# Kernel tuning notes

Measured on AMD Instinct MI355X. Metric: run time of the kernel, lower is better.

## Reference

```python
import jax, jax.numpy as jnp
import numpy as np

N = 50000
E = 800000
F_IN = 256
HID = 96
N_CLS = 32
NEG_SLOPE = 0.2


def setup_inputs() -> dict:
    key = jax.random.key(0)
    ks = jax.random.split(key, 10)
    x = jax.random.normal(ks[0], (N, F_IN), dtype=jnp.float32)
    edge_index = jax.random.randint(ks[1], (2, E), 0, N, dtype=jnp.int64)
    s1 = 1.0 / np.sqrt(F_IN)
    s2 = 1.0 / np.sqrt(HID)
    return {
        "x": x,
        "edge_index": edge_index,
        "W1": jax.random.normal(ks[2], (F_IN, HID), dtype=jnp.float32) * s1,
        "a1_src": jax.random.normal(ks[3], (HID,), dtype=jnp.float32) * s2,
        "a1_dst": jax.random.normal(ks[4], (HID,), dtype=jnp.float32) * s2,
        "b1": jnp.zeros((HID,), dtype=jnp.float32),
        "W2": jax.random.normal(ks[5], (HID, N_CLS), dtype=jnp.float32) * s2,
        "a2_src": jax.random.normal(ks[6], (N_CLS,), dtype=jnp.float32) * (1.0 / np.sqrt(N_CLS)),
        "a2_dst": jax.random.normal(ks[7], (N_CLS,), dtype=jnp.float32) * (1.0 / np.sqrt(N_CLS)),
        "b2": jnp.zeros((N_CLS,), dtype=jnp.float32),
    }


def _gat_conv(x, src, dst, W, a_src, a_dst, b, n_nodes):
    # single-head GATConv (PyG defaults), self-loops already in src/dst
    h = x @ W                                  # [N, out]
    alpha_src = h @ a_src                      # [N]
    alpha_dst = h @ a_dst                      # [N]
    e = alpha_src[src] + alpha_dst[dst]        # [E'] edge logits (msg j->i: dst groups)
    e = jnp.where(e > 0, e, NEG_SLOPE * e)     # leaky_relu
    # segment softmax over edges grouped by destination node
    m = jax.ops.segment_max(e, dst, num_segments=n_nodes)
    ex = jnp.exp(e - m[dst])
    denom = jax.ops.segment_sum(ex, dst, num_segments=n_nodes)
    alpha = ex / denom[dst]                    # [E']
    out = jax.ops.segment_sum(alpha[:, None] * h[src], dst, num_segments=n_nodes)
    return out + b


def reference(x, edge_index, W1, a1_src, a1_dst, b1, W2, a2_src, a2_dst, b2):
    loops = jnp.arange(N, dtype=edge_index.dtype)
    src = jnp.concatenate([edge_index[0], loops])
    dst = jnp.concatenate([edge_index[1], loops])
    h = _gat_conv(x, src, dst, W1, a1_src, a1_dst, b1, N)
    h = jax.nn.elu(h)
    # dropout omitted (eval mode, training=False)
    out = _gat_conv(h, src, dst, W2, a2_src, a2_dst, b2, N)
    return jax.nn.log_softmax(out, axis=1)
```

## Files before the change

kernel.cpp:

```cpp
#include <hip/hip_runtime.h>
#include <cstdint>
#include <cstddef>

#define NNODES 50000
#define NEDGES 800000
#define MEDGES (NEDGES + NNODES)
#define FIN    256
#define HID    96
#define NCLS   32
#define NEG_SLOPE 0.2f

#define NBUCK  391
#define BCAP   3072

typedef unsigned int uint32;
typedef __attribute__((ext_vector_type(8))) short short8;
typedef __attribute__((ext_vector_type(4))) float f32x4;

__device__ __forceinline__ ushort bf_round(float f) {
    uint32 u = __float_as_uint(f);
    u += 0x7FFFu + ((u >> 16) & 1u);
    return (ushort)(u >> 16);
}
__device__ __forceinline__ float bf_lo(uint32 u) { return __uint_as_float(u << 16); }
__device__ __forceinline__ float bf_hi(uint32 u) { return __uint_as_float(u & 0xFFFF0000u); }
__device__ __forceinline__ float lrelu(float t) { return (t > 0.f) ? t : NEG_SLOPE * t; }


__global__ __launch_bounds__(256) void bucket1_kernel(const int* __restrict__ ei,
                                                      int* __restrict__ gcount,
                                                      int2* __restrict__ staging) {
    __shared__ int hist[NBUCK];
    __shared__ int base_sh[NBUCK];
    for (int i = threadIdx.x; i < NBUCK; i += 256) hist[i] = 0;
    __syncthreads();

    int s[8], d[8], rk[8], bk[8];
    int e0 = blockIdx.x * 2048;
#pragma unroll
    for (int i = 0; i < 8; ++i) {
        int e = e0 + i * 256 + threadIdx.x;
        if (e < MEDGES) {
            if (e < NEDGES) { s[i] = ei[e]; d[i] = ei[NEDGES + e]; }
            else            { s[i] = e - NEDGES; d[i] = s[i]; }
            bk[i] = d[i] >> 7;
            rk[i] = atomicAdd(&hist[bk[i]], 1);
        } else bk[i] = -1;
    }
    __syncthreads();
    for (int i = threadIdx.x; i < NBUCK; i += 256) {
        int c = hist[i];
        base_sh[i] = c ? atomicAdd(&gcount[i], c) : 0;
    }
    __syncthreads();
#pragma unroll
    for (int i = 0; i < 8; ++i) {
        if (bk[i] >= 0) {
            int pos = base_sh[bk[i]] + rk[i];
            if (pos < BCAP)
                staging[(size_t)bk[i] * BCAP + pos] = make_int2(s[i], d[i]);
        }
    }
}

__global__ __launch_bounds__(512) void bscan_kernel(const int* __restrict__ gcount,
                                                    int* __restrict__ bbase) {
    __shared__ int sd[512];
    int t = threadIdx.x;
    int v = (t < NBUCK) ? gcount[t] : 0;
    sd[t] = v;
    __syncthreads();
    for (int off = 1; off < 512; off <<= 1) {
        int val = (t >= off) ? sd[t - off] : 0;
        __syncthreads();
        sd[t] += val;
        __syncthreads();
    }
    if (t < NBUCK) bbase[t] = sd[t] - v;
}

__global__ __launch_bounds__(256) void bucket2_kernel(const int2* __restrict__ staging,
                                                      const int* __restrict__ gcount,
                                                      const int* __restrict__ bbase,
                                                      int* __restrict__ rowptr,
                                                      int* __restrict__ esrc) {
    __shared__ int dcount[128];
    __shared__ int dincl[128];
    __shared__ int dexcl[128];
    __shared__ int fillc[128];

    const int b     = blockIdx.x;
    const int t     = threadIdx.x;
    const int cnt   = gcount[b];
    const int ebase = bbase[b];
    const int node0 = b << 7;
    const int2* st  = staging + (size_t)b * BCAP;

    for (int i = t; i < 128; i += 256) { dcount[i] = 0; fillc[i] = 0; }
    __syncthreads();

    for (int i = t; i < cnt; i += 256)
        atomicAdd(&dcount[st[i].y - node0], 1);
    __syncthreads();

    if (t < 128) dincl[t] = dcount[t];
    __syncthreads();
    for (int off = 1; off < 128; off <<= 1) {
        int val = (t >= off && t < 128) ? dincl[t - off] : 0;
        __syncthreads();
        if (t < 128) dincl[t] += val;
        __syncthreads();
    }
    if (t < 128) {
        int excl = dincl[t] - dcount[t];
        dexcl[t] = excl;
        int node = node0 + t;
        if (node < NNODES) rowptr[node] = ebase + excl;
    }
    if (b == NBUCK - 1 && t == 0) rowptr[NNODES] = MEDGES;
    __syncthreads();

    for (int i = t; i < cnt; i += 256) {
        int2 sd2 = st[i];
        int dd = sd2.y - node0;
        int r = atomicAdd(&fillc[dd], 1);
        esrc[ebase + dexcl[dd] + r] = sd2.x;
    }
}


__global__ __launch_bounds__(256) void packw1_kernel(const float* __restrict__ W1,
                                                     ushort* __restrict__ W1p) {
    for (int idx = threadIdx.x; idx < 6 * 8 * 64 * 8; idx += 256) {
        int j     = idx & 7;
        int lane  = (idx >> 3) & 63;
        int kstep = (idx >> 9) & 7;
        int ntile = idx >> 12;
        int k = kstep * 32 + ((lane >> 4) << 3) + j;
        int n = ntile * 16 + (lane & 15);
        W1p[idx] = bf_round(W1[(size_t)k * 96 + n]);
    }
}


__global__ __launch_bounds__(256) void gemm1_kernel(const float* __restrict__ x,
                                                    const ushort* __restrict__ W1p,
                                                    const float* __restrict__ a_src,
                                                    const float* __restrict__ a_dst,
                                                    ushort* __restrict__ h1,
                                                    float* __restrict__ as1,
                                                    float* __restrict__ ad1) {
    const int tid  = threadIdx.x;
    const int lane = tid & 63;
    const int wv   = tid >> 6;
    const int m    = lane & 15;
    const int quad = lane >> 4;
    const int node0 = blockIdx.x * 64;

    int arow = node0 + wv * 16 + m;
    if (arow >= NNODES) arow = NNODES - 1;
    const float* xr = x + (size_t)arow * FIN + quad * 8;

    const short8* Wp = (const short8*)W1p;

    f32x4 acc[6];
#pragma unroll
    for (int t = 0; t < 6; ++t) acc[t] = (f32x4){0.f, 0.f, 0.f, 0.f};

#pragma unroll
    for (int ks = 0; ks < 8; ++ks) {
        float4 v0 = *(const float4*)(xr + ks * 32);
        float4 v1 = *(const float4*)(xr + ks * 32 + 4);
        short8 a;
        a[0] = (short)bf_round(v0.x); a[1] = (short)bf_round(v0.y);
        a[2] = (short)bf_round(v0.z); a[3] = (short)bf_round(v0.w);
        a[4] = (short)bf_round(v1.x); a[5] = (short)bf_round(v1.y);
        a[6] = (short)bf_round(v1.z); a[7] = (short)bf_round(v1.w);
#pragma unroll
        for (int t = 0; t < 6; ++t) {
            short8 b = Wp[(t * 8 + ks) * 64 + lane];
            acc[t] = __builtin_amdgcn_mfma_f32_16x16x32_bf16(a, b, acc[t], 0, 0, 0);
        }
    }

    float as_reg[6], ad_reg[6];
#pragma unroll
    for (int t = 0; t < 6; ++t) {
        as_reg[t] = a_src[t * 16 + m];
        ad_reg[t] = a_dst[t * 16 + m];
    }

#pragma unroll
    for (int r = 0; r < 4; ++r) {
        int node = node0 + wv * 16 + quad * 4 + r;
        float ps = 0.f, pd = 0.f;
#pragma unroll
        for (int t = 0; t < 6; ++t) {
            ps += acc[t][r] * as_reg[t];
            pd += acc[t][r] * ad_reg[t];
        }
#pragma unroll
        for (int off = 1; off < 16; off <<= 1) {
            ps += __shfl_xor(ps, off);
            pd += __shfl_xor(pd, off);
        }
        if (node < NNODES) {
            ushort* hp = h1 + (size_t)node * 96 + m;
#pragma unroll
            for (int t = 0; t < 6; ++t) hp[t * 16] = bf_round(acc[t][r]);
            if (m == 0) { as1[node] = ps; ad1[node] = pd; }
        }
    }
}


__global__ __launch_bounds__(256) void gemm2_kernel(const float* __restrict__ y,
                                                    const float* __restrict__ W2,
                                                    const float* __restrict__ a_src,
                                                    const float* __restrict__ a_dst,
                                                    float* __restrict__ h2,
                                                    float* __restrict__ as2,
                                                    float* __restrict__ ad2) {
    __shared__ float ysT[96][66];
    __shared__ float red[2][4][64];

    const int tid  = threadIdx.x;
    const int lane = tid & 63;
    const int wid  = __builtin_amdgcn_readfirstlane(tid >> 6);
    const int node0 = blockIdx.x * 64;
    const int node  = node0 + lane;

    const int sr = tid & 63;
    const int sc = tid >> 6;
    int srow = node0 + sr; if (srow >= NNODES) srow = NNODES - 1;
    const float* yr = y + (size_t)srow * HID;

#pragma unroll
    for (int i = 0; i < 6; ++i) {
        int c = sc + 4 * i;
        float4 v = *(const float4*)(yr + 4 * c);
        int k = 4 * c;
        ysT[k + 0][sr] = v.x;
        ysT[k + 1][sr] = v.y;
        ysT[k + 2][sr] = v.z;
        ysT[k + 3][sr] = v.w;
    }
    __syncthreads();

    float acc[8];
#pragma unroll
    for (int j = 0; j < 8; ++j) acc[j] = 0.f;

#pragma unroll 4
    for (int k = 0; k < HID; ++k) {
        float xv = ysT[k][lane];
        const float* wr = W2 + (size_t)k * 32 + wid * 8;
        float w[8];
#pragma unroll
        for (int j = 0; j < 8; ++j) w[j] = wr[j];
#pragma unroll
        for (int j = 0; j < 8; ++j) acc[j] = fmaf(xv, w[j], acc[j]);
    }

    float ps = 0.f, pd = 0.f;
#pragma unroll
    for (int j = 0; j < 8; ++j) {
        ps += acc[j] * a_src[wid * 8 + j];
        pd += acc[j] * a_dst[wid * 8 + j];
    }
    red[0][wid][lane] = ps;
    red[1][wid][lane] = pd;

    if (node < NNODES) {
        float* hp = h2 + (size_t)node * NCLS + wid * 8;
        *(float4*)(hp + 0) = make_float4(acc[0], acc[1], acc[2], acc[3]);
        *(float4*)(hp + 4) = make_float4(acc[4], acc[5], acc[6], acc[7]);
    }
    __syncthreads();
    if (tid < 64) {
        int n2 = node0 + tid;
        if (n2 < NNODES) {
            as2[n2] = red[0][0][tid] + red[0][1][tid] + red[0][2][tid] + red[0][3][tid];
            ad2[n2] = red[1][0][tid] + red[1][1][tid] + red[1][2][tid] + red[1][3][tid];
        }
    }
}


__global__ __launch_bounds__(256) void agg96_kernel(const ushort* __restrict__ h,
                                                    const float* __restrict__ asrc,
                                                    const float* __restrict__ adst,
                                                    const float* __restrict__ bias,
                                                    const int* __restrict__ rowptr,
                                                    const int* __restrict__ esrc,
                                                    float* __restrict__ out) {
    int wave = threadIdx.x >> 6;
    int lane = threadIdx.x & 63;
    int i = blockIdx.x * 4 + wave;
    if (i >= NNODES) return;

    int start = rowptr[i], end = rowptr[i + 1];
    int deg = end - start;
    float ad = adst[i];
    int fl = (lane < 48) ? lane : 47;

    float acc0 = 0.f, acc1 = 0.f;

    if (deg <= 64) {
        int p = start + lane;
        bool valid = p < end;
        int s_reg = valid ? esrc[p] : 0;
        float e = -1e30f;
        if (valid) e = lrelu(asrc[s_reg] + ad);
        float mx = e;
#pragma unroll
        for (int off = 32; off; off >>= 1) mx = fmaxf(mx, __shfl_xor(mx, off));
        float ex = valid ? __expf(e - mx) : 0.f;
        float sum = ex;
#pragma unroll
        for (int off = 32; off; off >>= 1) sum += __shfl_xor(sum, off);
        float a_reg = ex / sum;

        int main_end = deg & ~3;
        for (int eb = 0; eb < main_end; eb += 4) {
            int s0 = __shfl(s_reg, eb + 0), s1 = __shfl(s_reg, eb + 1);
            int s2 = __shfl(s_reg, eb + 2), s3 = __shfl(s_reg, eb + 3);
            float a0 = __shfl(a_reg, eb + 0), a1 = __shfl(a_reg, eb + 1);
            float a2 = __shfl(a_reg, eb + 2), a3 = __shfl(a_reg, eb + 3);
            uint32 u0 = ((const uint32*)(h + (size_t)s0 * 96))[fl];
            uint32 u1 = ((const uint32*)(h + (size_t)s1 * 96))[fl];
            uint32 u2 = ((const uint32*)(h + (size_t)s2 * 96))[fl];
            uint32 u3 = ((const uint32*)(h + (size_t)s3 * 96))[fl];
            acc0 += a0 * bf_lo(u0) + a1 * bf_lo(u1) + a2 * bf_lo(u2) + a3 * bf_lo(u3);
            acc1 += a0 * bf_hi(u0) + a1 * bf_hi(u1) + a2 * bf_hi(u2) + a3 * bf_hi(u3);
        }
        for (int e2 = main_end; e2 < deg; ++e2) {
            int s = __shfl(s_reg, e2);
            float a = __shfl(a_reg, e2);
            uint32 u = ((const uint32*)(h + (size_t)s * 96))[fl];
            acc0 += a * bf_lo(u);
            acc1 += a * bf_hi(u);
        }
    } else {
        float mx = -1e30f;
        for (int p = start + lane; p < end; p += 64)
            mx = fmaxf(mx, lrelu(asrc[esrc[p]] + ad));
#pragma unroll
        for (int off = 32; off; off >>= 1) mx = fmaxf(mx, __shfl_xor(mx, off));
        float sum = 0.f;
        for (int p = start + lane; p < end; p += 64)
            sum += __expf(lrelu(asrc[esrc[p]] + ad) - mx);
#pragma unroll
        for (int off = 32; off; off >>= 1) sum += __shfl_xor(sum, off);
        float inv = 1.f / sum;
        for (int p = start; p < end; ++p) {
            int s = esrc[p];
            float a = __expf(lrelu(asrc[s] + ad) - mx) * inv;
            uint32 u = ((const uint32*)(h + (size_t)s * 96))[fl];
            acc0 += a * bf_lo(u);
            acc1 += a * bf_hi(u);
        }
    }

    if (lane < 48) {
        float v0 = acc0 + bias[2 * lane];
        v0 = (v0 > 0.f) ? v0 : expm1f(v0);
        float v1 = acc1 + bias[2 * lane + 1];
        v1 = (v1 > 0.f) ? v1 : expm1f(v1);
        *(float2*)(out + (size_t)i * 96 + 2 * lane) = make_float2(v0, v1);
    }
}


__global__ __launch_bounds__(256) void agg32_kernel(const float* __restrict__ h,
                                                    const float* __restrict__ asrc,
                                                    const float* __restrict__ adst,
                                                    const float* __restrict__ bias,
                                                    const int* __restrict__ rowptr,
                                                    const int* __restrict__ esrc,
                                                    float* __restrict__ out) {
    int wave = threadIdx.x >> 6;
    int lane = threadIdx.x & 63;
    int i = blockIdx.x * 4 + wave;
    if (i >= NNODES) return;

    int e2 = lane >> 5;
    int f  = lane & 31;

    int start = rowptr[i], end = rowptr[i + 1];
    int deg = end - start;
    float ad = adst[i];

    float acc = 0.f;

    if (deg <= 64) {
        int p = start + lane;
        bool valid = p < end;
        int s_reg = valid ? esrc[p] : 0;
        float e = -1e30f;
        if (valid) e = lrelu(asrc[s_reg] + ad);
        float mx = e;
#pragma unroll
        for (int off = 32; off; off >>= 1) mx = fmaxf(mx, __shfl_xor(mx, off));
        float ex = valid ? __expf(e - mx) : 0.f;
        float sum = ex;
#pragma unroll
        for (int off = 32; off; off >>= 1) sum += __shfl_xor(sum, off);
        float a_reg = ex / sum;

        int main_end = deg & ~7;
        for (int eb = 0; eb < main_end; eb += 8) {
            int idx0 = eb + e2, idx1 = eb + e2 + 2, idx2 = eb + e2 + 4, idx3 = eb + e2 + 6;
            int s0 = __shfl(s_reg, idx0), s1 = __shfl(s_reg, idx1);
            int s2 = __shfl(s_reg, idx2), s3 = __shfl(s_reg, idx3);
            float a0 = __shfl(a_reg, idx0), a1 = __shfl(a_reg, idx1);
            float a2 = __shfl(a_reg, idx2), a3 = __shfl(a_reg, idx3);
            float v0 = h[(size_t)s0 * 32 + f];
            float v1 = h[(size_t)s1 * 32 + f];
            float v2 = h[(size_t)s2 * 32 + f];
            float v3 = h[(size_t)s3 * 32 + f];
            acc += a0 * v0 + a1 * v1 + a2 * v2 + a3 * v3;
        }
        for (int e3 = main_end + e2; e3 < deg; e3 += 2) {
            int s = __shfl(s_reg, e3);
            float a = __shfl(a_reg, e3);
            acc += a * h[(size_t)s * 32 + f];
        }
        acc += __shfl_xor(acc, 32);
    } else {
        float mx = -1e30f;
        for (int p = start + lane; p < end; p += 64)
            mx = fmaxf(mx, lrelu(asrc[esrc[p]] + ad));
#pragma unroll
        for (int off = 32; off; off >>= 1) mx = fmaxf(mx, __shfl_xor(mx, off));
        float sum = 0.f;
        for (int p = start + lane; p < end; p += 64)
            sum += __expf(lrelu(asrc[esrc[p]] + ad) - mx);
#pragma unroll
        for (int off = 32; off; off >>= 1) sum += __shfl_xor(sum, off);
        float inv = 1.f / sum;
        for (int p = start + e2; p < end; p += 2) {
            int s = esrc[p];
            float a = __expf(lrelu(asrc[s] + ad) - mx) * inv;
            acc += a * h[(size_t)s * 32 + f];
        }
        acc += __shfl_xor(acc, 32);
    }

    float z = acc + bias[f];
    float m2 = z;
#pragma unroll
    for (int off = 16; off; off >>= 1) m2 = fmaxf(m2, __shfl_xor(m2, off));
    float ex = __expf(z - m2);
    float s2 = ex;
#pragma unroll
    for (int off = 16; off; off >>= 1) s2 += __shfl_xor(s2, off);
    if (lane < 32) out[(size_t)i * 32 + f] = z - m2 - logf(s2);
}


extern "C" void kernel_launch(void* const* d_in, const int* in_sizes, int n_in,
                              void* d_out, int out_size, void* d_ws, size_t ws_size,
                              hipStream_t stream) {
    const float* x   = (const float*)d_in[0];
    const int*   ei  = (const int*)d_in[1];
    const float* W1  = (const float*)d_in[2];
    const float* a1s = (const float*)d_in[3];
    const float* a1d = (const float*)d_in[4];
    const float* b1  = (const float*)d_in[5];
    const float* W2  = (const float*)d_in[6];
    const float* a2s = (const float*)d_in[7];
    const float* a2d = (const float*)d_in[8];
    const float* b2  = (const float*)d_in[9];
    float* out = (float*)d_out;

    size_t off = 0;
    auto alloc = [&](size_t bytes) {
        void* p = (char*)d_ws + off;
        off += (bytes + 255) & ~(size_t)255;
        return p;
    };
    ushort* h1    = (ushort*)alloc((size_t)NNODES * HID * 2);
    float* out1   = (float*)alloc((size_t)NNODES * HID * 4);
    int2* staging = (int2*)alloc((size_t)NBUCK * BCAP * 8);
    float* as1    = (float*)alloc((size_t)NNODES * 4);
    float* ad1    = (float*)alloc((size_t)NNODES * 4);
    float* as2    = (float*)alloc((size_t)NNODES * 4);
    float* ad2    = (float*)alloc((size_t)NNODES * 4);
    int*   rowptr = (int*)alloc((size_t)(NNODES + 1) * 4);
    int*   esrc   = (int*)alloc((size_t)MEDGES * 4);
    ushort* W1p   = (ushort*)alloc((size_t)6 * 8 * 64 * 8 * 2);
    int*   gcount = (int*)alloc((size_t)NBUCK * 4);
    int*   bbase  = (int*)alloc((size_t)NBUCK * 4);
    float* h2     = (float*)h1;

    hipMemsetAsync(gcount, 0, (size_t)NBUCK * 4, stream);

    const int nbB1   = (MEDGES + 2047) / 2048;
    const int nbGemm = (NNODES + 63) / 64;
    const int nbAgg  = (NNODES + 3) / 4;

    packw1_kernel<<<1, 256, 0, stream>>>(W1, W1p);
    bucket1_kernel<<<nbB1, 256, 0, stream>>>(ei, gcount, staging);
    bscan_kernel<<<1, 512, 0, stream>>>(gcount, bbase);
    bucket2_kernel<<<NBUCK, 256, 0, stream>>>(staging, gcount, bbase, rowptr, esrc);

    gemm1_kernel<<<nbGemm, 256, 0, stream>>>(x, W1p, a1s, a1d, h1, as1, ad1);
    agg96_kernel<<<nbAgg, 256, 0, stream>>>(h1, as1, ad1, b1, rowptr, esrc, out1);

    gemm2_kernel<<<nbGemm, 256, 0, stream>>>(out1, W2, a2s, a2d, h2, as2, ad2);
    agg32_kernel<<<nbAgg, 256, 0, stream>>>(h2, as2, ad2, b2, rowptr, esrc, out);
}
```

Baseline: 244.5 us.

## Store layer-1 output as bf16, use MFMA for GEMM2, stage edge weights in LDS

The first aggregation now writes its ELU output as packed bf16 instead of fp32, which halves that intermediate's write and read traffic. The second GEMM switches from a scalar LDS-transposed FMA loop to bf16 MFMA 16x16x32, with W2 pre-packed into fragment layout by the shared pack kernel. Both aggregation kernels place per-edge (src, alpha) pairs in LDS and read them with vector loads instead of repeated cross-lane shuffles, and agg96 unrolls its gather loop by 8. The cost is more bf16 rounding on the hidden activations and in the second GEMM.

```diff
diff --git a/kernel.cpp b/kernel.cpp
--- a/kernel.cpp
+++ b/kernel.cpp
@@ -22,9 +22,13 @@
     u += 0x7FFFu + ((u >> 16) & 1u);
     return (ushort)(u >> 16);
 }
+__device__ __forceinline__ uint32 pack_bf16x2(float a, float b) {
+    return (uint32)bf_round(a) | ((uint32)bf_round(b) << 16);
+}
 __device__ __forceinline__ float bf_lo(uint32 u) { return __uint_as_float(u << 16); }
 __device__ __forceinline__ float bf_hi(uint32 u) { return __uint_as_float(u & 0xFFFF0000u); }
 __device__ __forceinline__ float lrelu(float t) { return (t > 0.f) ? t : NEG_SLOPE * t; }
+__device__ __forceinline__ float af(int i) { return __int_as_float(i); }
 
 
 __global__ __launch_bounds__(256) void bucket1_kernel(const int* __restrict__ ei,
@@ -129,8 +133,10 @@
 }
 
 
-__global__ __launch_bounds__(256) void packw1_kernel(const float* __restrict__ W1,
-                                                     ushort* __restrict__ W1p) {
+__global__ __launch_bounds__(256) void packw_kernel(const float* __restrict__ W1,
+                                                    const float* __restrict__ W2,
+                                                    ushort* __restrict__ W1p,
+                                                    ushort* __restrict__ W2p) {
     for (int idx = threadIdx.x; idx < 6 * 8 * 64 * 8; idx += 256) {
         int j     = idx & 7;
         int lane  = (idx >> 3) & 63;
@@ -139,6 +145,15 @@
         int k = kstep * 32 + ((lane >> 4) << 3) + j;
         int n = ntile * 16 + (lane & 15);
         W1p[idx] = bf_round(W1[(size_t)k * 96 + n]);
+    }
+    for (int idx = threadIdx.x; idx < 2 * 3 * 64 * 8; idx += 256) {
+        int j     = idx & 7;
+        int lane  = (idx >> 3) & 63;
+        int kstep = (idx >> 9) % 3;
+        int ntile = (idx >> 9) / 3;
+        int k = kstep * 32 + ((lane >> 4) << 3) + j;
+        int n = ntile * 16 + (lane & 15);
+        W2p[idx] = bf_round(W2[(size_t)k * 32 + n]);
     }
 }
 
@@ -214,74 +229,65 @@
 }
 
 
-__global__ __launch_bounds__(256) void gemm2_kernel(const float* __restrict__ y,
-                                                    const float* __restrict__ W2,
+__global__ __launch_bounds__(256) void gemm2_kernel(const uint32* __restrict__ y48,
+                                                    const ushort* __restrict__ W2p,
                                                     const float* __restrict__ a_src,
                                                     const float* __restrict__ a_dst,
                                                     float* __restrict__ h2,
                                                     float* __restrict__ as2,
                                                     float* __restrict__ ad2) {
-    __shared__ float ysT[96][66];
-    __shared__ float red[2][4][64];
-
     const int tid  = threadIdx.x;
     const int lane = tid & 63;
-    const int wid  = __builtin_amdgcn_readfirstlane(tid >> 6);
+    const int wv   = tid >> 6;
+    const int m    = lane & 15;
+    const int quad = lane >> 4;
     const int node0 = blockIdx.x * 64;
-    const int node  = node0 + lane;
-
-    const int sr = tid & 63;
-    const int sc = tid >> 6;
-    int srow = node0 + sr; if (srow >= NNODES) srow = NNODES - 1;
-    const float* yr = y + (size_t)srow * HID;
-
-#pragma unroll
-    for (int i = 0; i < 6; ++i) {
-        int c = sc + 4 * i;
-        float4 v = *(const float4*)(yr + 4 * c);
-        int k = 4 * c;
-        ysT[k + 0][sr] = v.x;
-        ysT[k + 1][sr] = v.y;
-        ysT[k + 2][sr] = v.z;
-        ysT[k + 3][sr] = v.w;
-    }
-    __syncthreads();
-
-    float acc[8];
-#pragma unroll
-    for (int j = 0; j < 8; ++j) acc[j] = 0.f;
-
-#pragma unroll 4
-    for (int k = 0; k < HID; ++k) {
-        float xv = ysT[k][lane];
-        const float* wr = W2 + (size_t)k * 32 + wid * 8;
-        float w[8];
-#pragma unroll
-        for (int j = 0; j < 8; ++j) w[j] = wr[j];
-#pragma unroll
-        for (int j = 0; j < 8; ++j) acc[j] = fmaf(xv, w[j], acc[j]);
-    }
-
-    float ps = 0.f, pd = 0.f;
-#pragma unroll
-    for (int j = 0; j < 8; ++j) {
-        ps += acc[j] * a_src[wid * 8 + j];
-        pd += acc[j] * a_dst[wid * 8 + j];
-    }
-    red[0][wid][lane] = ps;
-    red[1][wid][lane] = pd;
-
-    if (node < NNODES) {
-        float* hp = h2 + (size_t)node * NCLS + wid * 8;
-        *(float4*)(hp + 0) = make_float4(acc[0], acc[1], acc[2], acc[3]);
-        *(float4*)(hp + 4) = make_float4(acc[4], acc[5], acc[6], acc[7]);
-    }
-    __syncthreads();
-    if (tid < 64) {
-        int n2 = node0 + tid;
-        if (n2 < NNODES) {
-            as2[n2] = red[0][0][tid] + red[0][1][tid] + red[0][2][tid] + red[0][3][tid];
-            ad2[n2] = red[1][0][tid] + red[1][1][tid] + red[1][2][tid] + red[1][3][tid];
+
+    int arow = node0 + wv * 16 + m;
+    if (arow >= NNODES) arow = NNODES - 1;
+    const short8* Ar = (const short8*)(y48 + (size_t)arow * 48);
+    const short8* Wp = (const short8*)W2p;
+
+    f32x4 acc[2];
+    acc[0] = (f32x4){0.f, 0.f, 0.f, 0.f};
+    acc[1] = (f32x4){0.f, 0.f, 0.f, 0.f};
+
+#pragma unroll
+    for (int ks = 0; ks < 3; ++ks) {
+        short8 a = Ar[ks * 4 + quad];
+#pragma unroll
+        for (int t = 0; t < 2; ++t) {
+            short8 b = Wp[(t * 3 + ks) * 64 + lane];
+            acc[t] = __builtin_amdgcn_mfma_f32_16x16x32_bf16(a, b, acc[t], 0, 0, 0);
+        }
+    }
+
+    float as_reg[2], ad_reg[2];
+#pragma unroll
+    for (int t = 0; t < 2; ++t) {
+        as_reg[t] = a_src[t * 16 + m];
+        ad_reg[t] = a_dst[t * 16 + m];
+    }
+
+#pragma unroll
+    for (int r = 0; r < 4; ++r) {
+        int node = node0 + wv * 16 + quad * 4 + r;
+        float ps = 0.f, pd = 0.f;
+#pragma unroll
+        for (int t = 0; t < 2; ++t) {
+            ps += acc[t][r] * as_reg[t];
+            pd += acc[t][r] * ad_reg[t];
+        }
+#pragma unroll
+        for (int off = 1; off < 16; off <<= 1) {
+            ps += __shfl_xor(ps, off);
+            pd += __shfl_xor(pd, off);
+        }
+        if (node < NNODES) {
+            float* hp = h2 + (size_t)node * 32 + m;
+            hp[0]  = acc[0][r];
+            hp[16] = acc[1][r];
+            if (m == 0) { as2[node] = ps; ad2[node] = pd; }
         }
     }
 }
@@ -293,7 +299,8 @@
                                                     const float* __restrict__ bias,
                                                     const int* __restrict__ rowptr,
                                                     const int* __restrict__ esrc,
-                                                    float* __restrict__ out) {
+                                                    uint32* __restrict__ out1b) {
+    __shared__ int2 sa[4][64];
     int wave = threadIdx.x >> 6;
     int lane = threadIdx.x & 63;
     int i = blockIdx.x * 4 + wave;
@@ -321,25 +328,44 @@
         for (int off = 32; off; off >>= 1) sum += __shfl_xor(sum, off);
         float a_reg = ex / sum;
 
-        int main_end = deg & ~3;
-        for (int eb = 0; eb < main_end; eb += 4) {
-            int s0 = __shfl(s_reg, eb + 0), s1 = __shfl(s_reg, eb + 1);
-            int s2 = __shfl(s_reg, eb + 2), s3 = __shfl(s_reg, eb + 3);
-            float a0 = __shfl(a_reg, eb + 0), a1 = __shfl(a_reg, eb + 1);
-            float a2 = __shfl(a_reg, eb + 2), a3 = __shfl(a_reg, eb + 3);
-            uint32 u0 = ((const uint32*)(h + (size_t)s0 * 96))[fl];
-            uint32 u1 = ((const uint32*)(h + (size_t)s1 * 96))[fl];
-            uint32 u2 = ((const uint32*)(h + (size_t)s2 * 96))[fl];
-            uint32 u3 = ((const uint32*)(h + (size_t)s3 * 96))[fl];
-            acc0 += a0 * bf_lo(u0) + a1 * bf_lo(u1) + a2 * bf_lo(u2) + a3 * bf_lo(u3);
-            acc1 += a0 * bf_hi(u0) + a1 * bf_hi(u1) + a2 * bf_hi(u2) + a3 * bf_hi(u3);
-        }
-        for (int e2 = main_end; e2 < deg; ++e2) {
-            int s = __shfl(s_reg, e2);
-            float a = __shfl(a_reg, e2);
-            uint32 u = ((const uint32*)(h + (size_t)s * 96))[fl];
-            acc0 += a * bf_lo(u);
-            acc1 += a * bf_hi(u);
+        sa[wave][lane] = make_int2(s_reg, __float_as_int(a_reg));
+        const int4* sap = (const int4*)&sa[wave][0];
+
+        int eb = 0;
+        for (; eb + 8 <= deg; eb += 8) {
+            int4 q0 = sap[(eb >> 1) + 0];
+            int4 q1 = sap[(eb >> 1) + 1];
+            int4 q2 = sap[(eb >> 1) + 2];
+            int4 q3 = sap[(eb >> 1) + 3];
+            uint32 u0 = ((const uint32*)(h + (size_t)q0.x * 96))[fl];
+            uint32 u1 = ((const uint32*)(h + (size_t)q0.z * 96))[fl];
+            uint32 u2 = ((const uint32*)(h + (size_t)q1.x * 96))[fl];
+            uint32 u3 = ((const uint32*)(h + (size_t)q1.z * 96))[fl];
+            uint32 u4 = ((const uint32*)(h + (size_t)q2.x * 96))[fl];
+            uint32 u5 = ((const uint32*)(h + (size_t)q2.z * 96))[fl];
+            uint32 u6 = ((const uint32*)(h + (size_t)q3.x * 96))[fl];
+            uint32 u7 = ((const uint32*)(h + (size_t)q3.z * 96))[fl];
+            acc0 += af(q0.y) * bf_lo(u0) + af(q0.w) * bf_lo(u1)
+                  + af(q1.y) * bf_lo(u2) + af(q1.w) * bf_lo(u3)
+                  + af(q2.y) * bf_lo(u4) + af(q2.w) * bf_lo(u5)
+                  + af(q3.y) * bf_lo(u6) + af(q3.w) * bf_lo(u7);
+            acc1 += af(q0.y) * bf_hi(u0) + af(q0.w) * bf_hi(u1)
+                  + af(q1.y) * bf_hi(u2) + af(q1.w) * bf_hi(u3)
+                  + af(q2.y) * bf_hi(u4) + af(q2.w) * bf_hi(u5)
+                  + af(q3.y) * bf_hi(u6) + af(q3.w) * bf_hi(u7);
+        }
+        for (; eb + 2 <= deg; eb += 2) {
+            int4 q = sap[eb >> 1];
+            uint32 u0 = ((const uint32*)(h + (size_t)q.x * 96))[fl];
+            uint32 u1 = ((const uint32*)(h + (size_t)q.z * 96))[fl];
+            acc0 += af(q.y) * bf_lo(u0) + af(q.w) * bf_lo(u1);
+            acc1 += af(q.y) * bf_hi(u0) + af(q.w) * bf_hi(u1);
+        }
+        if (eb < deg) {
+            int2 q = sa[wave][eb];
+            uint32 u = ((const uint32*)(h + (size_t)q.x * 96))[fl];
+            acc0 += af(q.y) * bf_lo(u);
+            acc1 += af(q.y) * bf_hi(u);
         }
     } else {
         float mx = -1e30f;
@@ -367,7 +393,7 @@
         v0 = (v0 > 0.f) ? v0 : expm1f(v0);
         float v1 = acc1 + bias[2 * lane + 1];
         v1 = (v1 > 0.f) ? v1 : expm1f(v1);
-        *(float2*)(out + (size_t)i * 96 + 2 * lane) = make_float2(v0, v1);
+        out1b[(size_t)i * 48 + lane] = pack_bf16x2(v0, v1);
     }
 }
 
@@ -379,6 +405,7 @@
                                                     const int* __restrict__ rowptr,
                                                     const int* __restrict__ esrc,
                                                     float* __restrict__ out) {
+    __shared__ int2 sa[4][64];
     int wave = threadIdx.x >> 6;
     int lane = threadIdx.x & 63;
     int i = blockIdx.x * 4 + wave;
@@ -408,23 +435,35 @@
         for (int off = 32; off; off >>= 1) sum += __shfl_xor(sum, off);
         float a_reg = ex / sum;
 
-        int main_end = deg & ~7;
-        for (int eb = 0; eb < main_end; eb += 8) {
-            int idx0 = eb + e2, idx1 = eb + e2 + 2, idx2 = eb + e2 + 4, idx3 = eb + e2 + 6;
-            int s0 = __shfl(s_reg, idx0), s1 = __shfl(s_reg, idx1);
-            int s2 = __shfl(s_reg, idx2), s3 = __shfl(s_reg, idx3);
-            float a0 = __shfl(a_reg, idx0), a1 = __shfl(a_reg, idx1);
-            float a2 = __shfl(a_reg, idx2), a3 = __shfl(a_reg, idx3);
+        sa[wave][lane] = make_int2(s_reg, __float_as_int(a_reg));
+        const int4* sap = (const int4*)&sa[wave][0];
+
+        int eb = 0;
+        for (; eb + 8 <= deg; eb += 8) {
+            int4 q0 = sap[(eb >> 1) + 0];
+            int4 q1 = sap[(eb >> 1) + 1];
+            int4 q2 = sap[(eb >> 1) + 2];
+            int4 q3 = sap[(eb >> 1) + 3];
+            int   s0 = e2 ? q0.z : q0.x;  float a0 = af(e2 ? q0.w : q0.y);
+            int   s1 = e2 ? q1.z : q1.x;  float a1 = af(e2 ? q1.w : q1.y);
+            int   s2 = e2 ? q2.z : q2.x;  float a2 = af(e2 ? q2.w : q2.y);
+            int   s3 = e2 ? q3.z : q3.x;  float a3 = af(e2 ? q3.w : q3.y);
             float v0 = h[(size_t)s0 * 32 + f];
             float v1 = h[(size_t)s1 * 32 + f];
             float v2 = h[(size_t)s2 * 32 + f];
             float v3 = h[(size_t)s3 * 32 + f];
             acc += a0 * v0 + a1 * v1 + a2 * v2 + a3 * v3;
         }
-        for (int e3 = main_end + e2; e3 < deg; e3 += 2) {
-            int s = __shfl(s_reg, e3);
-            float a = __shfl(a_reg, e3);
+        for (; eb + 2 <= deg; eb += 2) {
+            int4 q = sap[eb >> 1];
+            int   s = e2 ? q.z : q.x;
+            float a = af(e2 ? q.w : q.y);
             acc += a * h[(size_t)s * 32 + f];
+        }
+        if (eb < deg) {
+            int2 q = sa[wave][eb];
+            float a = (e2 == 0) ? af(q.y) : 0.f;
+            acc += a * h[(size_t)q.x * 32 + f];
         }
         acc += __shfl_xor(acc, 32);
     } else {
@@ -481,7 +520,7 @@
         return p;
     };
     ushort* h1    = (ushort*)alloc((size_t)NNODES * HID * 2);
-    float* out1   = (float*)alloc((size_t)NNODES * HID * 4);
+    uint32* out1b = (uint32*)alloc((size_t)NNODES * 48 * 4);
     int2* staging = (int2*)alloc((size_t)NBUCK * BCAP * 8);
     float* as1    = (float*)alloc((size_t)NNODES * 4);
     float* ad1    = (float*)alloc((size_t)NNODES * 4);
@@ -490,6 +529,7 @@
     int*   rowptr = (int*)alloc((size_t)(NNODES + 1) * 4);
     int*   esrc   = (int*)alloc((size_t)MEDGES * 4);
     ushort* W1p   = (ushort*)alloc((size_t)6 * 8 * 64 * 8 * 2);
+    ushort* W2p   = (ushort*)alloc((size_t)2 * 3 * 64 * 8 * 2);
     int*   gcount = (int*)alloc((size_t)NBUCK * 4);
     int*   bbase  = (int*)alloc((size_t)NBUCK * 4);
     float* h2     = (float*)h1;
@@ -500,14 +540,14 @@
     const int nbGemm = (NNODES + 63) / 64;
     const int nbAgg  = (NNODES + 3) / 4;
 
-    packw1_kernel<<<1, 256, 0, stream>>>(W1, W1p);
+    packw_kernel<<<1, 256, 0, stream>>>(W1, W2, W1p, W2p);
     bucket1_kernel<<<nbB1, 256, 0, stream>>>(ei, gcount, staging);
     bscan_kernel<<<1, 512, 0, stream>>>(gcount, bbase);
     bucket2_kernel<<<NBUCK, 256, 0, stream>>>(staging, gcount, bbase, rowptr, esrc);
 
     gemm1_kernel<<<nbGemm, 256, 0, stream>>>(x, W1p, a1s, a1d, h1, as1, ad1);
-    agg96_kernel<<<nbAgg, 256, 0, stream>>>(h1, as1, ad1, b1, rowptr, esrc, out1);
-
-    gemm2_kernel<<<nbGemm, 256, 0, stream>>>(out1, W2, a2s, a2d, h2, as2, ad2);
+    agg96_kernel<<<nbAgg, 256, 0, stream>>>(h1, as1, ad1, b1, rowptr, esrc, out1b);
+
+    gemm2_kernel<<<nbGemm, 256, 0, stream>>>(out1b, W2p, a2s, a2d, h2, as2, ad2);
     agg32_kernel<<<nbAgg, 256, 0, stream>>>(h2, as2, ad2, b2, rowptr, esrc, out);
 }
```

New measurement: 234.8 us. 3.9% less time.
